# Kernel tuning notes

Hardware: AMD Instinct MI355X
Metric: run time of the kernel (lower is better)

The kernel has to match this reference:

```python
import jax, jax.numpy as jnp
import numpy as np

SS, D, V = 64, 256, 10000
B, S = 16, 512


def setup_inputs() -> dict:
    key = jax.random.key(0)
    ks = jax.random.split(key, 7)
    scale = lambda fan_in: 1.0 / np.sqrt(fan_in)
    return {
        "x": jax.random.normal(ks[0], (B, S, D), dtype=jnp.float32),
        # nn.Linear(D, 4*ss): weight [4ss, D], bias [4ss]
        "Wxs_w": jax.random.uniform(ks[1], (4 * SS, D), jnp.float32, -scale(D), scale(D)),
        "Wxs_b": jax.random.uniform(ks[2], (4 * SS,), jnp.float32, -scale(D), scale(D)),
        # nn.Linear(ss, 4*ss)
        "Wss_w": jax.random.uniform(ks[3], (4 * SS, SS), jnp.float32, -scale(SS), scale(SS)),
        "Wss_b": jax.random.uniform(ks[4], (4 * SS,), jnp.float32, -scale(SS), scale(SS)),
        # nn.Linear(ss, V)
        "Wsy_w": jax.random.uniform(ks[5], (V, SS), jnp.float32, -scale(SS), scale(SS)),
        "Wsy_b": jax.random.uniform(ks[6], (V,), jnp.float32, -scale(SS), scale(SS)),
    }


def reference(x, Wxs_w, Wxs_b, Wss_w, Wss_b, Wsy_w, Wsy_b):
    b, s, _ = x.shape
    ss = Wss_w.shape[1]
    # Precompute input projections for all timesteps: [s, b, 4ss]
    xproj = jnp.einsum("bsd,kd->sbk", x, Wxs_w) + Wxs_b

    def step(carry, xp_t):
        h, c = carry
        comb = xp_t + h @ Wss_w.T + Wss_b  # [b, 4ss]
        f, i, g, o = jnp.split(comb, 4, axis=-1)
        f = jax.nn.sigmoid(f)
        i = jax.nn.sigmoid(i)
        o = jax.nn.sigmoid(o)
        g = jnp.tanh(g)
        c = c * f + i * g
        h = o * c  # NOTE: original code omits tanh(c) here; stay faithful
        return (h, c), h

    h0 = jnp.zeros((b, ss), dtype=x.dtype)
    c0 = jnp.zeros((b, ss), dtype=x.dtype)
    _, hs = jax.lax.scan(step, (h0, c0), xproj)  # hs: [s, b, ss]
    # Per-step vocab projection == batched projection of stacked hidden states
    y = jnp.einsum("sbh,vh->bsv", hs, Wsy_w) + Wsy_b  # [b, s, V]
    return y
```

## Files before the change

### kernel.cpp

```cpp
#include <hip/hip_runtime.h>

typedef unsigned short u16;
typedef unsigned int u32;

using short8 = __attribute__((ext_vector_type(8))) short;
using f32x4  = __attribute__((ext_vector_type(4))) float;

#define SSEQ 512
#define BB   16
#define DD   256
#define G4   256
#define SSZ  64
#define VV   10000
#define VPAD 10112
#define MALL 8192

#define OFF_XHI   0u
#define OFF_XLO   4194304u
#define OFF_WHI   8388608u
#define OFF_WLO   8519680u
#define OFF_WSY   8650752u
#define OFF_XPROJ 9945088u
#define OFF_HS    18333696u

__device__ __forceinline__ u16 f2bf(float f) {
  u32 u = __float_as_uint(f);
  u32 r = (u + 0x7fffu + ((u >> 16) & 1u)) >> 16;
  return (u16)r;
}
__device__ __forceinline__ float bf2f(u16 h) {
  return __uint_as_float(((u32)h) << 16);
}
__device__ __forceinline__ float sigm(float x) {
  float e = exp2f(-1.442695041f * x);
  return __builtin_amdgcn_rcpf(1.f + e);
}
__device__ __forceinline__ float tanh_fast(float x) {
  float xc = fminf(fmaxf(x, -20.f), 20.f);
  float z = exp2f(2.885390082f * xc);
  return (z - 1.f) * __builtin_amdgcn_rcpf(z + 1.f);
}

#define NX 2097152
#define NW 65536
#define NP 647168
__global__ void k0_convert(const float* __restrict__ x, const float* __restrict__ Wxs,
                           const float* __restrict__ Wsy,
                           u16* __restrict__ xhi, u16* __restrict__ xlo,
                           u16* __restrict__ whi, u16* __restrict__ wlo,
                           u16* __restrict__ wsyb) {
  int i = blockIdx.x * 256 + threadIdx.x;
  if (i < NX) {
    float v = x[i]; u16 h = f2bf(v);
    xhi[i] = h; xlo[i] = f2bf(v - bf2f(h));
  } else if (i < NX + NW) {
    int j = i - NX;
    float v = Wxs[j]; u16 h = f2bf(v);
    whi[j] = h; wlo[j] = f2bf(v - bf2f(h));
  } else if (i < NX + NW + NP) {
    int j = i - NX - NW;
    wsyb[j] = (j < VV * SSZ) ? f2bf(Wsy[j]) : (u16)0;
  }
}

__global__ __launch_bounds__(256) void k1_xproj(
    const u16* __restrict__ xhi, const u16* __restrict__ xlo,
    const u16* __restrict__ whi, const u16* __restrict__ wlo,
    const float* __restrict__ bias, float* __restrict__ xproj) {
  int bid = blockIdx.x;
  int mb = bid >> 1, nb = bid & 1;
  int tid = threadIdx.x, l = tid & 63, wid = tid >> 6;
  int wm = wid >> 1, wv = wid & 1;
  int m0 = mb * 128 + wm * 64, n0 = nb * 128 + wv * 64;
  int lr = l & 15, lg = l >> 4;

  f32x4 acc[4][4];
#pragma unroll
  for (int a = 0; a < 4; a++)
#pragma unroll
    for (int bq = 0; bq < 4; bq++) acc[a][bq] = (f32x4){0.f, 0.f, 0.f, 0.f};

#pragma unroll
  for (int p = 0; p < 3; p++) {
    const u16* A = (p == 1) ? xlo : xhi;
    const u16* B = (p == 2) ? wlo : whi;
#pragma unroll
    for (int ks = 0; ks < 8; ks++) {
      short8 af[4], bf_[4];
#pragma unroll
      for (int fm = 0; fm < 4; fm++)
        af[fm] = *(const short8*)(A + (size_t)(m0 + fm * 16 + lr) * 256 + ks * 32 + lg * 8);
#pragma unroll
      for (int fv = 0; fv < 4; fv++)
        bf_[fv] = *(const short8*)(B + (size_t)(n0 + fv * 16 + lr) * 256 + ks * 32 + lg * 8);
#pragma unroll
      for (int fm = 0; fm < 4; fm++)
#pragma unroll
        for (int fv = 0; fv < 4; fv++)
          acc[fm][fv] = __builtin_amdgcn_mfma_f32_16x16x32_bf16(af[fm], bf_[fv], acc[fm][fv], 0, 0, 0);
    }
  }
#pragma unroll
  for (int fv = 0; fv < 4; fv++) {
    int j = n0 + fv * 16 + lr;
    float bj = bias[j];
#pragma unroll
    for (int fm = 0; fm < 4; fm++)
#pragma unroll
      for (int r = 0; r < 4; r++) {
        int m = m0 + fm * 16 + lg * 4 + r;
        xproj[(size_t)m * 256 + j] = acc[fm][fv][r] + bj;
      }
  }
}

__global__ __launch_bounds__(256, 1) void k2_scan(
    const float* __restrict__ xproj, const float* __restrict__ Wss,
    const float* __restrict__ Wssb, u16* __restrict__ hsb) {
  __shared__ float lds[2][256];
  int b = blockIdx.x, tid = threadIdx.x, l = tid & 63;

  float wreg[64];
  const float4* wrow = (const float4*)(Wss + (size_t)tid * 64);
#pragma unroll
  for (int q = 0; q < 16; q++) {
    float4 w4 = wrow[q];
    wreg[4 * q + 0] = w4.x; wreg[4 * q + 1] = w4.y;
    wreg[4 * q + 2] = w4.z; wreg[4 * q + 3] = w4.w;
  }
  float bj = Wssb[tid];

  float hsg[64];
#pragma unroll
  for (int k = 0; k < 64; k++) hsg[k] = 0.f;
  float c = 0.f;

  const float* xpb = xproj + (size_t)b * SSEQ * 256 + tid;
  u16* hout = hsb + (size_t)b * SSEQ * 64 + l;
  float xp_next = xpb[0];

  for (int t = 0; t < SSEQ; t++) {
    float xp = xp_next;
    if (t + 1 < SSEQ) xp_next = xpb[(size_t)(t + 1) * 256];

    float a0 = xp + bj, a1 = 0.f, a2 = 0.f, a3 = 0.f;
#pragma unroll
    for (int k = 0; k < 16; k++) {
      a0 = fmaf(hsg[k],      wreg[k],      a0);
      a1 = fmaf(hsg[16 + k], wreg[16 + k], a1);
      a2 = fmaf(hsg[32 + k], wreg[32 + k], a2);
      a3 = fmaf(hsg[48 + k], wreg[48 + k], a3);
    }
    int buf = t & 1;
    lds[buf][tid] = (a0 + a1) + (a2 + a3);
    asm volatile("s_waitcnt lgkmcnt(0)\n\ts_barrier" ::: "memory");

    float fr = lds[buf][l];
    float ir = lds[buf][64 + l];
    float gr = lds[buf][128 + l];
    float orr = lds[buf][192 + l];

    float fg = sigm(fr), ig = sigm(ir), og = sigm(orr);
    float gg = tanh_fast(gr);
    c = fmaf(c, fg, ig * gg);
    float hn = og * c;

    if (tid < 64) hout[(size_t)t * 64] = f2bf(hn);

#pragma unroll
    for (int k = 0; k < 64; k++)
      hsg[k] = __uint_as_float(__builtin_amdgcn_readlane(__float_as_uint(hn), k));
  }
}

__global__ __launch_bounds__(256) void k3_y(
    const u16* __restrict__ hsb, const u16* __restrict__ wsyb,
    const float* __restrict__ bias, float* __restrict__ y) {
  int bid = blockIdx.x;
  int mb = bid / 79, vb = bid - mb * 79;
  int tid = threadIdx.x, l = tid & 63, wid = tid >> 6;
  int wm = wid >> 1, wv = wid & 1;
  int m0 = mb * 128 + wm * 64, v0 = vb * 128 + wv * 64;
  int lr = l & 15, lg = l >> 4;

  f32x4 acc[4][4];
#pragma unroll
  for (int a = 0; a < 4; a++)
#pragma unroll
    for (int bq = 0; bq < 4; bq++) acc[a][bq] = (f32x4){0.f, 0.f, 0.f, 0.f};

#pragma unroll
  for (int ks = 0; ks < 2; ks++) {
    short8 af[4], bf_[4];
#pragma unroll
    for (int fm = 0; fm < 4; fm++)
      af[fm] = *(const short8*)(hsb + (size_t)(m0 + fm * 16 + lr) * 64 + ks * 32 + lg * 8);
#pragma unroll
    for (int fv = 0; fv < 4; fv++)
      bf_[fv] = *(const short8*)(wsyb + (size_t)(v0 + fv * 16 + lr) * 64 + ks * 32 + lg * 8);
#pragma unroll
    for (int fm = 0; fm < 4; fm++)
#pragma unroll
      for (int fv = 0; fv < 4; fv++)
        acc[fm][fv] = __builtin_amdgcn_mfma_f32_16x16x32_bf16(af[fm], bf_[fv], acc[fm][fv], 0, 0, 0);
  }

#pragma unroll
  for (int fv = 0; fv < 4; fv++) {
    int v = v0 + fv * 16 + lr;
    bool ok = (v < VV);
    float bv = ok ? bias[v] : 0.f;
#pragma unroll
    for (int fm = 0; fm < 4; fm++)
#pragma unroll
      for (int r = 0; r < 4; r++) {
        int m = m0 + fm * 16 + lg * 4 + r;
        if (ok) y[(size_t)m * (size_t)VV + v] = acc[fm][fv][r] + bv;
      }
  }
}

extern "C" void kernel_launch(void* const* d_in, const int* in_sizes, int n_in,
                              void* d_out, int out_size, void* d_ws, size_t ws_size,
                              hipStream_t stream) {
  const float* x     = (const float*)d_in[0];
  const float* Wxs_w = (const float*)d_in[1];
  const float* Wxs_b = (const float*)d_in[2];
  const float* Wss_w = (const float*)d_in[3];
  const float* Wss_b = (const float*)d_in[4];
  const float* Wsy_w = (const float*)d_in[5];
  const float* Wsy_b = (const float*)d_in[6];
  float* y = (float*)d_out;
  char* ws = (char*)d_ws;

  u16*   xhi   = (u16*)(ws + OFF_XHI);
  u16*   xlo   = (u16*)(ws + OFF_XLO);
  u16*   whi   = (u16*)(ws + OFF_WHI);
  u16*   wlo   = (u16*)(ws + OFF_WLO);
  u16*   wsyb  = (u16*)(ws + OFF_WSY);
  float* xproj = (float*)(ws + OFF_XPROJ);
  u16*   hsb   = (u16*)(ws + OFF_HS);

  k0_convert<<<(NX + NW + NP) / 256, 256, 0, stream>>>(x, Wxs_w, Wsy_w, xhi, xlo, whi, wlo, wsyb);
  k1_xproj<<<128, 256, 0, stream>>>(xhi, xlo, whi, wlo, Wxs_b, xproj);
  k2_scan<<<16, 256, 0, stream>>>(xproj, Wss_w, Wss_b, hsb);
  k3_y<<<64 * 79, 256, 0, stream>>>(hsb, wsyb, Wsy_b, y);
}
```

Before: 339.9 us.

## Run LSTM scan with one wave per batch and packed FMA gates

The recurrent scan kernel now uses a single 64-lane wave per batch element. Each lane computes all four gate pre-activations for its hidden unit, using packed v_pk_fma_f32 over register-resident weights. The hidden state is exchanged through a small LDS buffer instead of a block barrier and 64 readlanes. This aims to cut per-step synchronization latency, but each lane now does four times the dot-product work and holds 256 weight floats in registers, which risks spilling and a longer serial chain.

Measured after the change: 573.5 us. 1.69x slower.

```diff
diff --git a/kernel.cpp b/kernel.cpp
--- a/kernel.cpp
+++ b/kernel.cpp
@@ -5,6 +5,7 @@
 
 using short8 = __attribute__((ext_vector_type(8))) short;
 using f32x4  = __attribute__((ext_vector_type(4))) float;
+using f32x2  = __attribute__((ext_vector_type(2))) float;
 
 #define SSEQ 512
 #define BB   16
@@ -39,6 +40,10 @@
   float xc = fminf(fmaxf(x, -20.f), 20.f);
   float z = exp2f(2.885390082f * xc);
   return (z - 1.f) * __builtin_amdgcn_rcpf(z + 1.f);
+}
+__device__ __forceinline__ f32x2 pkfma(f32x2 a, f32x2 b, f32x2 c) {
+  asm("v_pk_fma_f32 %0, %1, %2, %0" : "+v"(c) : "v"(a), "v"(b));
+  return c;
 }
 
 #define NX 2097152
@@ -114,62 +119,74 @@
   }
 }
 
-__global__ __launch_bounds__(256, 1) void k2_scan(
+__global__ __launch_bounds__(64, 1) void k2_scan(
     const float* __restrict__ xproj, const float* __restrict__ Wss,
     const float* __restrict__ Wssb, u16* __restrict__ hsb) {
-  __shared__ float lds[2][256];
-  int b = blockIdx.x, tid = threadIdx.x, l = tid & 63;
-
-  float wreg[64];
-  const float4* wrow = (const float4*)(Wss + (size_t)tid * 64);
-#pragma unroll
-  for (int q = 0; q < 16; q++) {
-    float4 w4 = wrow[q];
-    wreg[4 * q + 0] = w4.x; wreg[4 * q + 1] = w4.y;
-    wreg[4 * q + 2] = w4.z; wreg[4 * q + 3] = w4.w;
-  }
-  float bj = Wssb[tid];
-
-  float hsg[64];
-#pragma unroll
-  for (int k = 0; k < 64; k++) hsg[k] = 0.f;
+  __shared__ float hbuf[64];
+  int b = blockIdx.x, j = threadIdx.x;
+
+  f32x2 wf[32], wi[32], wg[32], wo[32];
+  {
+    const f32x2* pf = (const f32x2*)(Wss + (size_t)j * 64);
+    const f32x2* pi = (const f32x2*)(Wss + (size_t)(64 + j) * 64);
+    const f32x2* pg = (const f32x2*)(Wss + (size_t)(128 + j) * 64);
+    const f32x2* po = (const f32x2*)(Wss + (size_t)(192 + j) * 64);
+#pragma unroll
+    for (int q = 0; q < 32; q++) {
+      wf[q] = pf[q]; wi[q] = pi[q]; wg[q] = pg[q]; wo[q] = po[q];
+    }
+  }
+  float bf_ = Wssb[j], bi_ = Wssb[64 + j], bg_ = Wssb[128 + j], bo_ = Wssb[192 + j];
+
+  f32x4 h4[16];
+#pragma unroll
+  for (int q = 0; q < 16; q++) h4[q] = (f32x4){0.f, 0.f, 0.f, 0.f};
   float c = 0.f;
 
-  const float* xpb = xproj + (size_t)b * SSEQ * 256 + tid;
-  u16* hout = hsb + (size_t)b * SSEQ * 64 + l;
-  float xp_next = xpb[0];
+  const float* xpb = xproj + (size_t)b * SSEQ * 256;
+  u16* hout = hsb + (size_t)b * SSEQ * 64 + j;
+
+  float xf = xpb[j], xi = xpb[64 + j], xg = xpb[128 + j], xo = xpb[192 + j];
 
   for (int t = 0; t < SSEQ; t++) {
-    float xp = xp_next;
-    if (t + 1 < SSEQ) xp_next = xpb[(size_t)(t + 1) * 256];
-
-    float a0 = xp + bj, a1 = 0.f, a2 = 0.f, a3 = 0.f;
-#pragma unroll
-    for (int k = 0; k < 16; k++) {
-      a0 = fmaf(hsg[k],      wreg[k],      a0);
-      a1 = fmaf(hsg[16 + k], wreg[16 + k], a1);
-      a2 = fmaf(hsg[32 + k], wreg[32 + k], a2);
-      a3 = fmaf(hsg[48 + k], wreg[48 + k], a3);
-    }
-    int buf = t & 1;
-    lds[buf][tid] = (a0 + a1) + (a2 + a3);
-    asm volatile("s_waitcnt lgkmcnt(0)\n\ts_barrier" ::: "memory");
-
-    float fr = lds[buf][l];
-    float ir = lds[buf][64 + l];
-    float gr = lds[buf][128 + l];
-    float orr = lds[buf][192 + l];
-
-    float fg = sigm(fr), ig = sigm(ir), og = sigm(orr);
-    float gg = tanh_fast(gr);
+    float nf = 0.f, ni = 0.f, ng = 0.f, no_ = 0.f;
+    if (t + 1 < SSEQ) {
+      const float* xn = xpb + (size_t)(t + 1) * 256;
+      nf = xn[j]; ni = xn[64 + j]; ng = xn[128 + j]; no_ = xn[192 + j];
+    }
+
+    f32x2 af = (f32x2){bf_ + xf, 0.f};
+    f32x2 ai = (f32x2){bi_ + xi, 0.f};
+    f32x2 ag = (f32x2){bg_ + xg, 0.f};
+    f32x2 ao = (f32x2){bo_ + xo, 0.f};
+#pragma unroll
+    for (int q = 0; q < 16; q++) {
+      f32x2 hA = (f32x2){h4[q][0], h4[q][1]};
+      f32x2 hB = (f32x2){h4[q][2], h4[q][3]};
+      af = pkfma(hA, wf[2 * q], af);     af = pkfma(hB, wf[2 * q + 1], af);
+      ai = pkfma(hA, wi[2 * q], ai);     ai = pkfma(hB, wi[2 * q + 1], ai);
+      ag = pkfma(hA, wg[2 * q], ag);     ag = pkfma(hB, wg[2 * q + 1], ag);
+      ao = pkfma(hA, wo[2 * q], ao);     ao = pkfma(hB, wo[2 * q + 1], ao);
+    }
+    float vf = af[0] + af[1];
+    float vi = ai[0] + ai[1];
+    float vg = ag[0] + ag[1];
+    float vo = ao[0] + ao[1];
+
+    float fg = sigm(vf), ig = sigm(vi), og = sigm(vo);
+    float gg = tanh_fast(vg);
     c = fmaf(c, fg, ig * gg);
     float hn = og * c;
 
-    if (tid < 64) hout[(size_t)t * 64] = f2bf(hn);
-
-#pragma unroll
-    for (int k = 0; k < 64; k++)
-      hsg[k] = __uint_as_float(__builtin_amdgcn_readlane(__float_as_uint(hn), k));
+    hout[(size_t)t * 64] = f2bf(hn);
+
+    hbuf[j] = hn;
+    asm volatile("s_waitcnt lgkmcnt(0)" ::: "memory");
+    const f32x4* hb4 = (const f32x4*)hbuf;
+#pragma unroll
+    for (int q = 0; q < 16; q++) h4[q] = hb4[q];
+
+    xf = nf; xi = ni; xg = ng; xo = no_;
   }
 }
 
@@ -243,6 +260,6 @@
 
   k0_convert<<<(NX + NW + NP) / 256, 256, 0, stream>>>(x, Wxs_w, Wsy_w, xhi, xlo, whi, wlo, wsyb);
   k1_xproj<<<128, 256, 0, stream>>>(xhi, xlo, whi, wlo, Wxs_b, xproj);
-  k2_scan<<<16, 256, 0, stream>>>(xproj, Wss_w, Wss_b, hsb);
+  k2_scan<<<16, 64, 0, stream>>>(xproj, Wss_w, Wss_b, hsb);
   k3_y<<<64 * 79, 256, 0, stream>>>(hsb, wsyb, Wsy_b, y);
 }
```

## Spread LSTM gate activations across waves and vectorize vocab projection stores

Applied to the files above, without the earlier changes.

The scan kernel now has each of the four waves apply its own gate's nonlinearity before the LDS exchange, instead of wave-level redundant computation of all four. It broadcasts h through LDS as float4 loads rather than 64 readlanes, and uses packed v_pk_fma_f32 for the recurrent dot product. Hidden states are staged in LDS and written out in bulk at the end. The output GEMM swaps its MFMA operands so each lane holds four consecutive vocab columns, which allows float4 bias loads and float4 stores. The scan now needs two barriers per step instead of one and uses 64KB of LDS for staging.

Result: faster. 331.8 us (-2.4%).

```diff
diff --git a/kernel.cpp b/kernel.cpp
--- a/kernel.cpp
+++ b/kernel.cpp
@@ -5,6 +5,7 @@
 
 using short8 = __attribute__((ext_vector_type(8))) short;
 using f32x4  = __attribute__((ext_vector_type(4))) float;
+using f32x2  = __attribute__((ext_vector_type(2))) float;
 
 #define SSEQ 512
 #define BB   16
@@ -39,6 +40,10 @@
   float xc = fminf(fmaxf(x, -20.f), 20.f);
   float z = exp2f(2.885390082f * xc);
   return (z - 1.f) * __builtin_amdgcn_rcpf(z + 1.f);
+}
+__device__ __forceinline__ f32x2 pkfma(f32x2 a, f32x2 b, f32x2 c) {
+  asm("v_pk_fma_f32 %0, %1, %2, %0" : "+v"(c) : "v"(a), "v"(b));
+  return c;
 }
 
 #define NX 2097152
@@ -117,60 +122,74 @@
 __global__ __launch_bounds__(256, 1) void k2_scan(
     const float* __restrict__ xproj, const float* __restrict__ Wss,
     const float* __restrict__ Wssb, u16* __restrict__ hsb) {
-  __shared__ float lds[2][256];
-  int b = blockIdx.x, tid = threadIdx.x, l = tid & 63;
-
-  float wreg[64];
-  const float4* wrow = (const float4*)(Wss + (size_t)tid * 64);
-#pragma unroll
-  for (int q = 0; q < 16; q++) {
-    float4 w4 = wrow[q];
-    wreg[4 * q + 0] = w4.x; wreg[4 * q + 1] = w4.y;
-    wreg[4 * q + 2] = w4.z; wreg[4 * q + 3] = w4.w;
-  }
-  float bj = Wssb[tid];
-
-  float hsg[64];
-#pragma unroll
-  for (int k = 0; k < 64; k++) hsg[k] = 0.f;
+  __shared__ float gact[4][64];
+  __shared__ float hbuf[64];
+  __shared__ u16 hstage[SSEQ][64];
+
+  int b = blockIdx.x, tid = threadIdx.x;
+  int w = tid >> 6, j = tid & 63;
+
+  f32x2 wr[32];
+  const f32x2* pw = (const f32x2*)(Wss + (size_t)(w * 64 + j) * 64);
+#pragma unroll
+  for (int q = 0; q < 32; q++) wr[q] = pw[q];
+  float bg = Wssb[w * 64 + j];
+
+  f32x4 h4[16];
+#pragma unroll
+  for (int q = 0; q < 16; q++) h4[q] = (f32x4){0.f, 0.f, 0.f, 0.f};
   float c = 0.f;
 
-  const float* xpb = xproj + (size_t)b * SSEQ * 256 + tid;
-  u16* hout = hsb + (size_t)b * SSEQ * 64 + l;
-  float xp_next = xpb[0];
+  const float* xpb = xproj + (size_t)b * SSEQ * 256 + w * 64 + j;
+  float xp0 = xpb[0];
+  float xp1 = xpb[256];
 
   for (int t = 0; t < SSEQ; t++) {
-    float xp = xp_next;
-    if (t + 1 < SSEQ) xp_next = xpb[(size_t)(t + 1) * 256];
-
-    float a0 = xp + bj, a1 = 0.f, a2 = 0.f, a3 = 0.f;
-#pragma unroll
-    for (int k = 0; k < 16; k++) {
-      a0 = fmaf(hsg[k],      wreg[k],      a0);
-      a1 = fmaf(hsg[16 + k], wreg[16 + k], a1);
-      a2 = fmaf(hsg[32 + k], wreg[32 + k], a2);
-      a3 = fmaf(hsg[48 + k], wreg[48 + k], a3);
-    }
-    int buf = t & 1;
-    lds[buf][tid] = (a0 + a1) + (a2 + a3);
+    float xp2 = (t + 2 < SSEQ) ? xpb[(size_t)(t + 2) * 256] : 0.f;
+
+    f32x2 a0 = (f32x2){bg + xp0, 0.f};
+    f32x2 a1 = (f32x2){0.f, 0.f};
+    f32x2 a2 = (f32x2){0.f, 0.f};
+    f32x2 a3 = (f32x2){0.f, 0.f};
+#pragma unroll
+    for (int q = 0; q < 8; q++) {
+      f32x2 hA0 = (f32x2){h4[2 * q][0], h4[2 * q][1]};
+      f32x2 hB0 = (f32x2){h4[2 * q][2], h4[2 * q][3]};
+      f32x2 hA1 = (f32x2){h4[2 * q + 1][0], h4[2 * q + 1][1]};
+      f32x2 hB1 = (f32x2){h4[2 * q + 1][2], h4[2 * q + 1][3]};
+      a0 = pkfma(hA0, wr[4 * q + 0], a0);
+      a1 = pkfma(hB0, wr[4 * q + 1], a1);
+      a2 = pkfma(hA1, wr[4 * q + 2], a2);
+      a3 = pkfma(hB1, wr[4 * q + 3], a3);
+    }
+    float a = (a0[0] + a0[1]) + (a1[0] + a1[1]) + ((a2[0] + a2[1]) + (a3[0] + a3[1]));
+
+    float act = (w == 2) ? tanh_fast(a) : sigm(a);
+    gact[w][j] = act;
     asm volatile("s_waitcnt lgkmcnt(0)\n\ts_barrier" ::: "memory");
 
-    float fr = lds[buf][l];
-    float ir = lds[buf][64 + l];
-    float gr = lds[buf][128 + l];
-    float orr = lds[buf][192 + l];
-
-    float fg = sigm(fr), ig = sigm(ir), og = sigm(orr);
-    float gg = tanh_fast(gr);
+    float fg = gact[0][j], ig = gact[1][j], gg = gact[2][j], og = gact[3][j];
     c = fmaf(c, fg, ig * gg);
     float hn = og * c;
 
-    if (tid < 64) hout[(size_t)t * 64] = f2bf(hn);
-
-#pragma unroll
-    for (int k = 0; k < 64; k++)
-      hsg[k] = __uint_as_float(__builtin_amdgcn_readlane(__float_as_uint(hn), k));
-  }
+    if (w == 0) {
+      hbuf[j] = hn;
+      hstage[t][j] = f2bf(hn);
+    }
+    asm volatile("s_waitcnt lgkmcnt(0)\n\ts_barrier" ::: "memory");
+
+    const f32x4* hb = (const f32x4*)hbuf;
+#pragma unroll
+    for (int q = 0; q < 16; q++) h4[q] = hb[q];
+
+    xp0 = xp1; xp1 = xp2;
+  }
+
+  __syncthreads();
+  const uint4* src = (const uint4*)hstage;
+  uint4* dst = (uint4*)(hsb + (size_t)b * SSEQ * 64);
+#pragma unroll
+  for (int i = 0; i < 16; i++) dst[tid + 256 * i] = src[tid + 256 * i];
 }
 
 __global__ __launch_bounds__(256) void k3_y(
@@ -199,24 +218,29 @@
     for (int fv = 0; fv < 4; fv++)
       bf_[fv] = *(const short8*)(wsyb + (size_t)(v0 + fv * 16 + lr) * 64 + ks * 32 + lg * 8);
 #pragma unroll
-    for (int fm = 0; fm < 4; fm++)
-#pragma unroll
-      for (int fv = 0; fv < 4; fv++)
-        acc[fm][fv] = __builtin_amdgcn_mfma_f32_16x16x32_bf16(af[fm], bf_[fv], acc[fm][fv], 0, 0, 0);
+    for (int fv = 0; fv < 4; fv++)
+#pragma unroll
+      for (int fm = 0; fm < 4; fm++)
+        acc[fv][fm] = __builtin_amdgcn_mfma_f32_16x16x32_bf16(bf_[fv], af[fm], acc[fv][fm], 0, 0, 0);
   }
 
 #pragma unroll
   for (int fv = 0; fv < 4; fv++) {
-    int v = v0 + fv * 16 + lr;
-    bool ok = (v < VV);
-    float bv = ok ? bias[v] : 0.f;
-#pragma unroll
-    for (int fm = 0; fm < 4; fm++)
-#pragma unroll
-      for (int r = 0; r < 4; r++) {
-        int m = m0 + fm * 16 + lg * 4 + r;
-        if (ok) y[(size_t)m * (size_t)VV + v] = acc[fm][fv][r] + bv;
+    int vb4 = v0 + fv * 16 + lg * 4;
+    bool ok = (vb4 + 3) < VV;
+    float4 bv = ok ? *(const float4*)(bias + vb4) : float4{0.f, 0.f, 0.f, 0.f};
+#pragma unroll
+    for (int fm = 0; fm < 4; fm++) {
+      int m = m0 + fm * 16 + lr;
+      if (ok) {
+        float4 o;
+        o.x = acc[fv][fm][0] + bv.x;
+        o.y = acc[fv][fm][1] + bv.y;
+        o.z = acc[fv][fm][2] + bv.z;
+        o.w = acc[fv][fm][3] + bv.w;
+        *(float4*)(y + (size_t)m * (size_t)VV + vb4) = o;
       }
+    }
   }
 }
 
```
